# Performance work log

Measured on AMD Instinct MI355X. Metric: run time of the kernel, lower is better.

Reference implementation:

```python
import jax, jax.numpy as jnp
import numpy as np

B, T, F, H, O = 128, 512, 512, 1024, 1


def setup_inputs() -> dict:
    key = jax.random.key(0)
    ks = jax.random.split(key, 11)
    s_ih1 = 1.0 / np.sqrt(H)
    return {
        "x": jax.random.normal(ks[0], (B, T, F), dtype=jnp.float32),
        # LSTMCell params, torch layout: weight_ih [4H, in], weight_hh [4H, H]
        "W_ih1": jax.random.uniform(ks[1], (4 * H, F), jnp.float32, -s_ih1, s_ih1),
        "W_hh1": jax.random.uniform(ks[2], (4 * H, H), jnp.float32, -s_ih1, s_ih1),
        "b_ih1": jax.random.uniform(ks[3], (4 * H,), jnp.float32, -s_ih1, s_ih1),
        "b_hh1": jax.random.uniform(ks[4], (4 * H,), jnp.float32, -s_ih1, s_ih1),
        "W_ih2": jax.random.uniform(ks[5], (4 * H, H), jnp.float32, -s_ih1, s_ih1),
        "W_hh2": jax.random.uniform(ks[6], (4 * H, H), jnp.float32, -s_ih1, s_ih1),
        "b_ih2": jax.random.uniform(ks[7], (4 * H,), jnp.float32, -s_ih1, s_ih1),
        "b_hh2": jax.random.uniform(ks[8], (4 * H,), jnp.float32, -s_ih1, s_ih1),
        "W_lin": jax.random.uniform(ks[9], (O, H), jnp.float32, -s_ih1, s_ih1),
        "b_lin": jax.random.uniform(ks[10], (O,), jnp.float32, -s_ih1, s_ih1),
    }


def _lstm_cell(x_t, h, c, W_ih, W_hh, b_ih, b_hh):
    # gates: [B, 4H]; torch gate order i, f, g, o
    gates = x_t @ W_ih.T + b_ih + h @ W_hh.T + b_hh
    i, f, g, o = jnp.split(gates, 4, axis=-1)
    i, f, o = jax.nn.sigmoid(i), jax.nn.sigmoid(f), jax.nn.sigmoid(o)
    g = jnp.tanh(g)
    c_new = f * c + i * g
    h_new = o * jnp.tanh(c_new)
    return h_new, c_new


def reference(x, W_ih1, W_hh1, b_ih1, b_hh1, W_ih2, W_hh2, b_ih2, b_hh2, W_lin, b_lin):
    B_, dtype = x.shape[0], x.dtype
    zeros = jnp.zeros((B_, H), dtype=dtype)
    init = (zeros, zeros, zeros, zeros)  # h1, c1, h2, c2

    def step(carry, x_t):
        h1, c1, h2, c2 = carry
        h1, c1 = _lstm_cell(x_t, h1, c1, W_ih1, W_hh1, b_ih1, b_hh1)
        h2, c2 = _lstm_cell(h1, h2, c2, W_ih2, W_hh2, b_ih2, b_hh2)
        return (h1, c1, h2, c2), None

    (h1, c1, h2, c2), _ = jax.lax.scan(step, init, jnp.swapaxes(x, 0, 1))
    # linear applied to the last timestep's h2 only (loop overwrites output)
    return h2 @ W_lin.T + b_lin
```

## Files before the change

kernel.cpp:

```cpp
#include <hip/hip_runtime.h>

#define Bb  128
#define Tt  512
#define Ff  512
#define Hh  1024
#define BH  (Bb*Hh)
#define WGS 512
#define NBLK 192

#define OFF_H1   0u
#define OFF_H2   524288u
#define OFF_H2F  1048576u
#define OFF_BAR  1572864u
#define OFF_PB   1576960u
#define OFF_WB   5771264u
#define OFF_XB   9965568u
#define WS_MIN   9965568u
#define WS_FULL  77074432u

typedef __attribute__((ext_vector_type(8))) short short8;
typedef __attribute__((ext_vector_type(4))) float f32x4;

__device__ __forceinline__ short f2bf(float f){
  union { float fv; unsigned u; } v; v.fv = f;
  unsigned r = v.u + 0x7fffu + ((v.u >> 16) & 1u);
  return (short)(r >> 16);
}

__device__ __forceinline__ f32x4 mfma16(short8 a, short8 b, f32x4 c){
  return __builtin_amdgcn_mfma_f32_16x16x32_bf16(a, b, c, 0, 0, 0);
}

#define CLDH(dst, base, OFFB) \
  asm volatile("global_load_dwordx4 %0, %1, off offset:" #OFFB " sc0 sc1" \
               : "=v"(dst) : "v"(base) : "memory")
#define CLDF(dst, base, OFFB) \
  asm volatile("global_load_dwordx4 %0, %1, off offset:" #OFFB " sc0 sc1" \
               : "=v"(dst) : "v"(base) : "memory")
#define CSTF(base, val, OFFB) \
  asm volatile("global_store_dwordx4 %0, %1, off offset:" #OFFB " sc0 sc1" \
               :: "v"(base), "v"(val) : "memory")

__device__ __forceinline__ void st_bf16_coh(short* p, short v){
  asm volatile("global_store_short %0, %1, off sc0 sc1"
               :: "v"(p), "v"((unsigned)(unsigned short)v) : "memory");
}

__global__ void __launch_bounds__(WGS) conv_wih1(const float* __restrict__ W,
                                                 short* __restrict__ Wb){
  const int fi   = blockIdx.x * WGS + threadIdx.x;
  const int nt   = fi >> 10;
  const int ch   = (fi >> 6) & 15;
  const int lane = fi & 63;
  const int grow = nt*16 + (lane & 15);
  const int k    = (ch << 5) + ((lane >> 4) << 3);
  const float* s = W + (size_t)grow * Ff + k;
  short8 v;
  #pragma unroll
  for (int e = 0; e < 8; ++e) v[e] = f2bf(s[e]);
  *(short8*)(Wb + (size_t)fi * 8) = v;
}

__global__ void __launch_bounds__(WGS) conv_x(const float* __restrict__ xf,
                                              short* __restrict__ xb){
  const size_t i = ((size_t)blockIdx.x * WGS + threadIdx.x) * 8;
  float4 u0 = *(const float4*)(xf + i);
  float4 u1 = *(const float4*)(xf + i + 4);
  short8 v;
  v[0]=f2bf(u0.x); v[1]=f2bf(u0.y); v[2]=f2bf(u0.z); v[3]=f2bf(u0.w);
  v[4]=f2bf(u1.x); v[5]=f2bf(u1.y); v[6]=f2bf(u1.z); v[7]=f2bf(u1.w);
  *(short8*)(xb + i) = v;
}

__global__ void __launch_bounds__(WGS) lstm_spec(
    const float* __restrict__ x, const short* __restrict__ xb, int use_xb,
    const float* __restrict__ Whh1,
    const float* __restrict__ bih1, const float* __restrict__ bhh1,
    const float* __restrict__ Wih2, const float* __restrict__ Whh2,
    const float* __restrict__ bih2, const float* __restrict__ bhh2,
    const short* __restrict__ Wb,
    short* __restrict__ h1buf, short* __restrict__ h2buf,
    float* __restrict__ PB, float* __restrict__ h2f32,
    unsigned* __restrict__ bar)
{
  extern __shared__ short LW[];
  const int bid = blockIdx.x, tid = threadIdx.x;
  const int grp = bid >> 6;
  const int cu  = bid & 63;
  const int c0  = cu << 4;

  const float* Wsrc = (grp == 0) ? Whh1 : (grp == 1) ? Wih2 : Whh2;
  for (int fi = tid; fi < 8192; fi += WGS){
    const int g = fi >> 11, ch = (fi >> 6) & 31, ln = fi & 63;
    const int grow = (g << 10) + c0 + (ln & 15);
    const int k    = (ch << 5) + ((ln >> 4) << 3);
    const float* s = Wsrc + (size_t)grow * Hh + k;
    short8 v;
    #pragma unroll
    for (int e = 0; e < 8; ++e) v[e] = f2bf(s[e]);
    *(short8*)(LW + (size_t)fi * 8) = v;
  }
  __syncthreads();

  const int lane = tid & 63, wv = tid >> 6;
  const int r0   = (wv << 4) + (lane & 15);
  const int kg8  = (lane >> 4) << 3;
  const int j    = lane & 15;
  const int bb   = (wv << 4) + ((lane >> 4) << 2);
  const int gcol = c0 + j;
  const int slot = bid & 7;

  float bsum[4], cst[4];
  #pragma unroll
  for (int g = 0; g < 4; ++g)
    bsum[g] = (grp == 0) ? bih1[(g << 10) + gcol] + bhh1[(g << 10) + gcol]
            : (grp == 2) ? bih2[(g << 10) + gcol] + bhh2[(g << 10) + gcol] : 0.f;
  #pragma unroll
  for (int r = 0; r < 4; ++r) cst[r] = 0.f;

  for (int p = 0; p <= Tt + 1; ++p){
    if (grp == 0 && p < Tt){
      f32x4 acc[4] = {{0,0,0,0},{0,0,0,0},{0,0,0,0},{0,0,0,0}};
      const short* hp  = h1buf + ((p + 1) & 1) * BH + r0 * Hh + kg8;
      const short* xbp = xb + ((size_t)r0 * Tt + p) * Ff + kg8;
      const float* xfp = x  + ((size_t)r0 * Tt + p) * Ff + kg8;
      #pragma unroll
      for (int cb = 0; cb < 4; ++cb){
        const short* hc = hp + (cb << 8);
        short8 hb[8];
        CLDH(hb[0], hc, 0);   CLDH(hb[1], hc, 64);  CLDH(hb[2], hc, 128);
        CLDH(hb[3], hc, 192); CLDH(hb[4], hc, 256); CLDH(hb[5], hc, 320);
        CLDH(hb[6], hc, 384); CLDH(hb[7], hc, 448);
        short8 xa[4];
        if (use_xb){
          #pragma unroll
          for (int u = 0; u < 4; ++u)
            xa[u] = *(const short8*)(xbp + (cb << 7) + (u << 5));
        } else {
          #pragma unroll
          for (int u = 0; u < 4; ++u){
            float4 u0 = *(const float4*)(xfp + (cb << 7) + (u << 5));
            float4 u1 = *(const float4*)(xfp + (cb << 7) + (u << 5) + 4);
            xa[u][0]=f2bf(u0.x); xa[u][1]=f2bf(u0.y); xa[u][2]=f2bf(u0.z); xa[u][3]=f2bf(u0.w);
            xa[u][4]=f2bf(u1.x); xa[u][5]=f2bf(u1.y); xa[u][6]=f2bf(u1.z); xa[u][7]=f2bf(u1.w);
          }
        }
        asm volatile("s_waitcnt vmcnt(0)" ::: "memory");
        __builtin_amdgcn_sched_barrier(0);
        #pragma unroll
        for (int g = 0; g < 4; ++g){
          #pragma unroll
          for (int u = 0; u < 8; ++u)
            acc[g] = mfma16(hb[u], *(const short8*)(LW + ((size_t)(((g<<5)+(cb<<3)+u)<<6) + lane)*8), acc[g]);
          #pragma unroll
          for (int u = 0; u < 4; ++u)
            acc[g] = mfma16(xa[u], *(const short8*)(Wb + ((size_t)((((g<<6)+cu)<<4)+(cb<<2)+u)*64 + lane)*8), acc[g]);
        }
      }
      short* hw = h1buf + (p & 1) * BH;
      #pragma unroll
      for (int r = 0; r < 4; ++r){
        float gi = acc[0][r] + bsum[0], gf = acc[1][r] + bsum[1];
        float gg = acc[2][r] + bsum[2], go = acc[3][r] + bsum[3];
        float iv = 1.f/(1.f+__expf(-gi)), fv = 1.f/(1.f+__expf(-gf));
        float gv = tanhf(gg),             ov = 1.f/(1.f+__expf(-go));
        cst[r] = fv * cst[r] + iv * gv;
        st_bf16_coh(hw + (size_t)(bb + r) * Hh + gcol, f2bf(ov * tanhf(cst[r])));
      }
    } else if (grp == 1 && p >= 1 && p <= Tt){
      f32x4 acc[4] = {{0,0,0,0},{0,0,0,0},{0,0,0,0},{0,0,0,0}};
      const short* hp = h1buf + ((p + 1) & 1) * BH + r0 * Hh + kg8;
      #pragma unroll
      for (int cb = 0; cb < 4; ++cb){
        const short* hc = hp + (cb << 8);
        short8 hb[8];
        CLDH(hb[0], hc, 0);   CLDH(hb[1], hc, 64);  CLDH(hb[2], hc, 128);
        CLDH(hb[3], hc, 192); CLDH(hb[4], hc, 256); CLDH(hb[5], hc, 320);
        CLDH(hb[6], hc, 384); CLDH(hb[7], hc, 448);
        asm volatile("s_waitcnt vmcnt(0)" ::: "memory");
        __builtin_amdgcn_sched_barrier(0);
        #pragma unroll
        for (int g = 0; g < 4; ++g)
          #pragma unroll
          for (int u = 0; u < 8; ++u)
            acc[g] = mfma16(hb[u], *(const short8*)(LW + ((size_t)(((g<<5)+(cb<<3)+u)<<6) + lane)*8), acc[g]);
      }
      float* pw = PB + (((size_t)((p + 1) & 1) * 64 + cu) * 8 + wv) * 1024 + lane * 16;
      CSTF(pw, acc[0], 0); CSTF(pw, acc[1], 16); CSTF(pw, acc[2], 32); CSTF(pw, acc[3], 48);
    } else if (grp == 2 && p >= 2){
      const float* pr = PB + (((size_t)(p & 1) * 64 + cu) * 8 + wv) * 1024 + lane * 16;
      f32x4 acc[4];
      CLDF(acc[0], pr, 0); CLDF(acc[1], pr, 16); CLDF(acc[2], pr, 32); CLDF(acc[3], pr, 48);
      const short* hp = h2buf + ((p + 1) & 1) * BH + r0 * Hh + kg8;
      #pragma unroll
      for (int cb = 0; cb < 4; ++cb){
        const short* hc = hp + (cb << 8);
        short8 hb[8];
        CLDH(hb[0], hc, 0);   CLDH(hb[1], hc, 64);  CLDH(hb[2], hc, 128);
        CLDH(hb[3], hc, 192); CLDH(hb[4], hc, 256); CLDH(hb[5], hc, 320);
        CLDH(hb[6], hc, 384); CLDH(hb[7], hc, 448);
        asm volatile("s_waitcnt vmcnt(0)" ::: "memory");
        __builtin_amdgcn_sched_barrier(0);
        #pragma unroll
        for (int g = 0; g < 4; ++g)
          #pragma unroll
          for (int u = 0; u < 8; ++u)
            acc[g] = mfma16(hb[u], *(const short8*)(LW + ((size_t)(((g<<5)+(cb<<3)+u)<<6) + lane)*8), acc[g]);
      }
      short* hw = h2buf + (p & 1) * BH;
      #pragma unroll
      for (int r = 0; r < 4; ++r){
        float gi = acc[0][r] + bsum[0], gf = acc[1][r] + bsum[1];
        float gg = acc[2][r] + bsum[2], go = acc[3][r] + bsum[3];
        float iv = 1.f/(1.f+__expf(-gi)), fv = 1.f/(1.f+__expf(-gf));
        float gv = tanhf(gg),             ov = 1.f/(1.f+__expf(-go));
        cst[r] = fv * cst[r] + iv * gv;
        float hv = ov * tanhf(cst[r]);
        st_bf16_coh(hw + (size_t)(bb + r) * Hh + gcol, f2bf(hv));
        if (p == Tt + 1) h2f32[(size_t)(bb + r) * Hh + gcol] = hv;
      }
    }

    __syncthreads();
    if (tid == 0){
      unsigned prev = __hip_atomic_fetch_add(bar + (slot << 6), 1u,
                        __ATOMIC_RELAXED, __HIP_MEMORY_SCOPE_AGENT);
      if (prev == (unsigned)(24 * (p + 1)) - 1u)
        __hip_atomic_fetch_add(bar + 768, 1u,
                        __ATOMIC_RELAXED, __HIP_MEMORY_SCOPE_AGENT);
      while (__hip_atomic_load(bar + 768,
                        __ATOMIC_RELAXED, __HIP_MEMORY_SCOPE_AGENT)
             < (unsigned)(8 * (p + 1)))
        __builtin_amdgcn_s_sleep(2);
    }
    __syncthreads();
  }
}

__global__ void final_linear(const float* __restrict__ h2, const float* __restrict__ Wl,
                             const float* __restrict__ bl, float* __restrict__ out){
  __shared__ float red[256];
  const int b = blockIdx.x, t = threadIdx.x;
  float s = 0.f;
  for (int k = t; k < Hh; k += 256) s += h2[(size_t)b * Hh + k] * Wl[k];
  red[t] = s; __syncthreads();
  for (int off = 128; off > 0; off >>= 1){ if (t < off) red[t] += red[t + off]; __syncthreads(); }
  if (t == 0) out[b] = red[0] + bl[0];
}

extern "C" void kernel_launch(void* const* d_in, const int* in_sizes, int n_in,
                              void* d_out, int out_size, void* d_ws, size_t ws_size,
                              hipStream_t stream) {
  (void)in_sizes; (void)n_in; (void)out_size;
  const float* x    = (const float*)d_in[0];
  const float* Wih1 = (const float*)d_in[1];
  const float* Whh1 = (const float*)d_in[2];
  const float* bih1 = (const float*)d_in[3];
  const float* bhh1 = (const float*)d_in[4];
  const float* Wih2 = (const float*)d_in[5];
  const float* Whh2 = (const float*)d_in[6];
  const float* bih2 = (const float*)d_in[7];
  const float* bhh2 = (const float*)d_in[8];
  const float* Wlin = (const float*)d_in[9];
  const float* blin = (const float*)d_in[10];
  float* out = (float*)d_out;

  if (ws_size < WS_MIN) return;
  const int use_xb = (ws_size >= WS_FULL) ? 1 : 0;

  char* ws = (char*)d_ws;
  short*    h1buf = (short*)(ws + OFF_H1);
  short*    h2buf = (short*)(ws + OFF_H2);
  float*    h2f32 = (float*)(ws + OFF_H2F);
  unsigned* bar   = (unsigned*)(ws + OFF_BAR);
  float*    PB    = (float*)(ws + OFF_PB);
  short*    Wb    = (short*)(ws + OFF_WB);
  short*    xb    = (short*)(ws + OFF_XB);

  hipMemsetAsync(d_ws, 0, OFF_WB, stream);
  conv_wih1<<<dim3(512), dim3(WGS), 0, stream>>>(Wih1, Wb);
  if (use_xb) conv_x<<<dim3(8192), dim3(WGS), 0, stream>>>(x, xb);
  hipFuncSetAttribute(reinterpret_cast<const void*>(lstm_spec),
                      hipFuncAttributeMaxDynamicSharedMemorySize, 131072);
  lstm_spec<<<dim3(NBLK), dim3(WGS), 131072, stream>>>(
      x, use_xb ? xb : Wb, use_xb, Whh1, bih1, bhh1, Wih2, Whh2, bih2, bhh2,
      Wb, h1buf, h2buf, PB, h2f32, bar);
  final_linear<<<dim3(Bb), dim3(256), 0, stream>>>(h2f32, Wlin, blin, out);
}
```

Before: 11.72 ms.

## Restructure persistent LSTM into four-group pipeline with register-resident weights and 32x32 MFMA

Adds a fourth block group that computes the x·W_ih1 projection one step ahead into a double-buffered PBX array, so it comes off the layer-1 critical path. Weights now sit in registers as bf16 fragments, and hidden states are staged through swizzled LDS for 32x32x16 MFMAs. A K-split with an LDS reduction is added, and gate columns are interleaved so each thread handles all four gates of one unit. The cost is an extra pipeline phase, more global scratch traffic for the preactivations, high register pressure, and mandatory full workspace use.

```diff
diff --git a/kernel.cpp b/kernel.cpp
--- a/kernel.cpp
+++ b/kernel.cpp
@@ -6,59 +6,54 @@
 #define Hh  1024
 #define BH  (Bb*Hh)
 #define WGS 512
-#define NBLK 192
+#define NBLK 256
+#define NPH 515
+#define PBH (128*4096)
 
 #define OFF_H1   0u
 #define OFF_H2   524288u
 #define OFF_H2F  1048576u
 #define OFF_BAR  1572864u
 #define OFF_PB   1576960u
-#define OFF_WB   5771264u
+#define OFF_PBX  5771264u
 #define OFF_XB   9965568u
-#define WS_MIN   9965568u
-#define WS_FULL  77074432u
+#define WS_NEED  77074432u
 
 typedef __attribute__((ext_vector_type(8))) short short8;
 typedef __attribute__((ext_vector_type(4))) float f32x4;
+typedef __attribute__((ext_vector_type(16))) float f32x16;
 
 __device__ __forceinline__ short f2bf(float f){
   union { float fv; unsigned u; } v; v.fv = f;
   unsigned r = v.u + 0x7fffu + ((v.u >> 16) & 1u);
   return (short)(r >> 16);
 }
-
-__device__ __forceinline__ f32x4 mfma16(short8 a, short8 b, f32x4 c){
-  return __builtin_amdgcn_mfma_f32_16x16x32_bf16(a, b, c, 0, 0, 0);
-}
-
-#define CLDH(dst, base, OFFB) \
-  asm volatile("global_load_dwordx4 %0, %1, off offset:" #OFFB " sc0 sc1" \
-               : "=v"(dst) : "v"(base) : "memory")
-#define CLDF(dst, base, OFFB) \
-  asm volatile("global_load_dwordx4 %0, %1, off offset:" #OFFB " sc0 sc1" \
-               : "=v"(dst) : "v"(base) : "memory")
-#define CSTF(base, val, OFFB) \
-  asm volatile("global_store_dwordx4 %0, %1, off offset:" #OFFB " sc0 sc1" \
-               :: "v"(base), "v"(val) : "memory")
-
-__device__ __forceinline__ void st_bf16_coh(short* p, short v){
+__device__ __forceinline__ float sigm(float x){ return 1.f/(1.f+__expf(-x)); }
+
+__device__ __forceinline__ f32x16 mfma32(short8 a, short8 b, f32x16 c){
+  return __builtin_amdgcn_mfma_f32_32x32x16_bf16(a, b, c, 0, 0, 0);
+}
+
+__device__ __forceinline__ short8 scld8(const short* p){
+  short8 d;
+  asm volatile("global_load_dwordx4 %0, %1, off sc0 sc1" : "=v"(d) : "v"(p) : "memory");
+  return d;
+}
+__device__ __forceinline__ f32x4 scldf4(const float* p){
+  f32x4 d;
+  asm volatile("global_load_dwordx4 %0, %1, off sc0 sc1" : "=v"(d) : "v"(p) : "memory");
+  return d;
+}
+__device__ __forceinline__ void sstf4(float* p, f32x4 v){
+  asm volatile("global_store_dwordx4 %0, %1, off sc0 sc1" :: "v"(p), "v"(v) : "memory");
+}
+__device__ __forceinline__ void ssth(short* p, short v){
   asm volatile("global_store_short %0, %1, off sc0 sc1"
                :: "v"(p), "v"((unsigned)(unsigned short)v) : "memory");
 }
-
-__global__ void __launch_bounds__(WGS) conv_wih1(const float* __restrict__ W,
-                                                 short* __restrict__ Wb){
-  const int fi   = blockIdx.x * WGS + threadIdx.x;
-  const int nt   = fi >> 10;
-  const int ch   = (fi >> 6) & 15;
-  const int lane = fi & 63;
-  const int grow = nt*16 + (lane & 15);
-  const int k    = (ch << 5) + ((lane >> 4) << 3);
-  const float* s = W + (size_t)grow * Ff + k;
-  short8 v;
-  #pragma unroll
-  for (int e = 0; e < 8; ++e) v[e] = f2bf(s[e]);
-  *(short8*)(Wb + (size_t)fi * 8) = v;
+__device__ __forceinline__ void drain_vm(){
+  asm volatile("s_waitcnt vmcnt(0)" ::: "memory");
+  __builtin_amdgcn_sched_barrier(0);
 }
 
 __global__ void __launch_bounds__(WGS) conv_x(const float* __restrict__ xf,
@@ -72,166 +67,206 @@
   *(short8*)(xb + i) = v;
 }
 
-__global__ void __launch_bounds__(WGS) lstm_spec(
-    const float* __restrict__ x, const short* __restrict__ xb, int use_xb,
-    const float* __restrict__ Whh1,
+__global__ void __launch_bounds__(WGS, 2) lstm4(
+    const short* __restrict__ xb,
+    const float* __restrict__ Wih1, const float* __restrict__ Whh1,
     const float* __restrict__ bih1, const float* __restrict__ bhh1,
     const float* __restrict__ Wih2, const float* __restrict__ Whh2,
     const float* __restrict__ bih2, const float* __restrict__ bhh2,
-    const short* __restrict__ Wb,
-    short* __restrict__ h1buf, short* __restrict__ h2buf,
-    float* __restrict__ PB, float* __restrict__ h2f32,
-    unsigned* __restrict__ bar)
+    short* __restrict__ h1, short* __restrict__ h2,
+    float* __restrict__ PB, float* __restrict__ PBX,
+    float* __restrict__ h2f32, unsigned* __restrict__ bar)
 {
-  extern __shared__ short LW[];
+  extern __shared__ char lds[];
+  float* F  = (float*)lds;
+  float* Lb = (float*)(lds + 131072);
+
   const int bid = blockIdx.x, tid = threadIdx.x;
   const int grp = bid >> 6;
   const int cu  = bid & 63;
-  const int c0  = cu << 4;
-
-  const float* Wsrc = (grp == 0) ? Whh1 : (grp == 1) ? Wih2 : Whh2;
-  for (int fi = tid; fi < 8192; fi += WGS){
-    const int g = fi >> 11, ch = (fi >> 6) & 31, ln = fi & 63;
-    const int grow = (g << 10) + c0 + (ln & 15);
-    const int k    = (ch << 5) + ((ln >> 4) << 3);
-    const float* s = Wsrc + (size_t)grow * Hh + k;
+  const int c0h = cu << 4;
+  const int lane = tid & 63, wv = tid >> 6;
+  const int tc = lane & 31, hi = lane >> 5;
+  const int slot = bid & 7;
+
+  const int cth = wv & 1;
+  const int kh  = (wv >> 1) & 1;
+  const int rh  = wv >> 2;
+  const int xrt = wv >> 1;
+
+  if (tid < 64){
+    const int hc = tid >> 2, g = tid & 3;
+    float v = 0.f;
+    if (grp == 0) v = bih1[(g<<10) + c0h + hc] + bhh1[(g<<10) + c0h + hc];
+    if (grp == 2) v = bih2[(g<<10) + c0h + hc] + bhh2[(g<<10) + c0h + hc];
+    Lb[tid] = v;
+  }
+
+  const float* Wsrc = (grp==0) ? Whh1 : (grp==1) ? Wih2 : (grp==2) ? Whh2 : Wih1;
+  const int Kdim = (grp==3) ? Ff : Hh;
+  const int kb0  = (grp==3) ? 0 : kh*512;
+  const int wrow = (tc&3)*Hh + c0h + cth*8 + (tc>>2);
+  short8 bfr[32];
+  #pragma unroll
+  for (int f = 0; f < 32; ++f){
+    const float* s = Wsrc + (size_t)wrow*Kdim + kb0 + f*16 + hi*8;
+    float4 u0 = *(const float4*)(s);
+    float4 u1 = *(const float4*)(s + 4);
     short8 v;
-    #pragma unroll
-    for (int e = 0; e < 8; ++e) v[e] = f2bf(s[e]);
-    *(short8*)(LW + (size_t)fi * 8) = v;
+    v[0]=f2bf(u0.x); v[1]=f2bf(u0.y); v[2]=f2bf(u0.z); v[3]=f2bf(u0.w);
+    v[4]=f2bf(u1.x); v[5]=f2bf(u1.y); v[6]=f2bf(u1.z); v[7]=f2bf(u1.w);
+    bfr[f] = v;
   }
   __syncthreads();
 
-  const int lane = tid & 63, wv = tid >> 6;
-  const int r0   = (wv << 4) + (lane & 15);
-  const int kg8  = (lane >> 4) << 3;
-  const int j    = lane & 15;
-  const int bb   = (wv << 4) + ((lane >> 4) << 2);
-  const int gcol = c0 + j;
-  const int slot = bid & 7;
-
-  float bsum[4], cst[4];
-  #pragma unroll
-  for (int g = 0; g < 4; ++g)
-    bsum[g] = (grp == 0) ? bih1[(g << 10) + gcol] + bhh1[(g << 10) + gcol]
-            : (grp == 2) ? bih2[(g << 10) + gcol] + bhh2[(g << 10) + gcol] : 0.f;
-  #pragma unroll
-  for (int r = 0; r < 4; ++r) cst[r] = 0.f;
-
-  for (int p = 0; p <= Tt + 1; ++p){
-    if (grp == 0 && p < Tt){
-      f32x4 acc[4] = {{0,0,0,0},{0,0,0,0},{0,0,0,0},{0,0,0,0}};
-      const short* hp  = h1buf + ((p + 1) & 1) * BH + r0 * Hh + kg8;
-      const short* xbp = xb + ((size_t)r0 * Tt + p) * Ff + kg8;
-      const float* xfp = x  + ((size_t)r0 * Tt + p) * Ff + kg8;
+  float cst[4] = {0.f, 0.f, 0.f, 0.f};
+  const int swz = (lane & 31) << 4;
+
+  for (int p = 0; p < NPH; ++p){
+    const bool act = (grp==0) ? (p>=1 && p<=512)
+                   : (grp==1) ? (p>=2 && p<=513)
+                   : (grp==2) ? (p>=3 && p<=514)
+                   :            (p < 512);
+    const short* sh = (grp==2) ? (h2 + (p&1)*BH) : (h1 + (p&1)*BH);
+
+    f32x4 pre[4] = {{0,0,0,0},{0,0,0,0},{0,0,0,0},{0,0,0,0}};
+    if (act && (grp == 0 || grp == 2)){
+      const float* src = (grp == 0) ? (PBX + (size_t)((p+1)&1)*PBH)
+                                    : (PB  + (size_t)((p+1)&1)*PBH);
       #pragma unroll
-      for (int cb = 0; cb < 4; ++cb){
-        const short* hc = hp + (cb << 8);
-        short8 hb[8];
-        CLDH(hb[0], hc, 0);   CLDH(hb[1], hc, 64);  CLDH(hb[2], hc, 128);
-        CLDH(hb[3], hc, 192); CLDH(hb[4], hc, 256); CLDH(hb[5], hc, 320);
-        CLDH(hb[6], hc, 384); CLDH(hb[7], hc, 448);
-        short8 xa[4];
-        if (use_xb){
-          #pragma unroll
-          for (int u = 0; u < 4; ++u)
-            xa[u] = *(const short8*)(xbp + (cb << 7) + (u << 5));
+      for (int s4 = 0; s4 < 4; ++s4){
+        const int id = (s4<<9) + tid;
+        pre[s4] = scldf4(src + (size_t)(id>>4)*4096 + ((c0h + (id&15))<<2));
+      }
+    }
+
+    f32x16 a0, a1;
+    #pragma unroll
+    for (int i = 0; i < 16; ++i){ a0[i] = 0.f; a1[i] = 0.f; }
+
+    #pragma unroll
+    for (int r = 0; r < 2; ++r){
+      if (act){
+        if (grp != 3){
+          #pragma unroll
+          for (int buf = 0; buf < 2; ++buf){
+            const int kq = 2*buf + r;
+            short8 t[8];
+            #pragma unroll
+            for (int i = 0; i < 8; ++i){
+              const int u = (i<<9) + tid;
+              t[i] = scld8(sh + (size_t)(u>>5)*Hh + kq*256 + (u&31)*8);
+            }
+            drain_vm();
+            #pragma unroll
+            for (int i = 0; i < 8; ++i){
+              const int u = (i<<9) + tid;
+              *(short8*)(lds + buf*65536 + (((u<<4)) ^ ((((u>>5)&31))<<4))) = t[i];
+            }
+          }
         } else {
-          #pragma unroll
-          for (int u = 0; u < 4; ++u){
-            float4 u0 = *(const float4*)(xfp + (cb << 7) + (u << 5));
-            float4 u1 = *(const float4*)(xfp + (cb << 7) + (u << 5) + 4);
-            xa[u][0]=f2bf(u0.x); xa[u][1]=f2bf(u0.y); xa[u][2]=f2bf(u0.z); xa[u][3]=f2bf(u0.w);
-            xa[u][4]=f2bf(u1.x); xa[u][5]=f2bf(u1.y); xa[u][6]=f2bf(u1.z); xa[u][7]=f2bf(u1.w);
-          }
-        }
-        asm volatile("s_waitcnt vmcnt(0)" ::: "memory");
-        __builtin_amdgcn_sched_barrier(0);
+          short8 t[8];
+          #pragma unroll
+          for (int i = 0; i < 8; ++i){
+            const int u = (i<<9) + tid;
+            t[i] = *(const short8*)(xb + ((size_t)(u>>5)*Tt + p)*Ff + r*256 + (u&31)*8);
+          }
+          #pragma unroll
+          for (int i = 0; i < 8; ++i){
+            const int u = (i<<9) + tid;
+            *(short8*)(lds + r*65536 + (((u<<4)) ^ ((((u>>5)&31))<<4))) = t[i];
+          }
+        }
+      }
+      __syncthreads();
+      if (act){
+        if (grp != 3){
+          const int row0 = rh*64 + (lane & 31);
+          const char* b0 = lds + kh*65536 + row0*512;
+          const char* b1 = b0 + 32*512;
+          #pragma unroll
+          for (int ci = 0; ci < 16; ++ci){
+            const int ko = (((ci<<5) | (hi<<4)) ^ swz);
+            short8 A0 = *(const short8*)(b0 + ko);
+            short8 A1 = *(const short8*)(b1 + ko);
+            a0 = mfma32(A0, bfr[r*16+ci], a0);
+            a1 = mfma32(A1, bfr[r*16+ci], a1);
+          }
+        } else {
+          const int row0 = xrt*32 + (lane & 31);
+          const char* b0 = lds + r*65536 + row0*512;
+          #pragma unroll
+          for (int ci = 0; ci < 16; ++ci){
+            const int ko = (((ci<<5) | (hi<<4)) ^ swz);
+            short8 A0 = *(const short8*)(b0 + ko);
+            a0 = mfma32(A0, bfr[r*16+ci], a0);
+          }
+        }
+      }
+      __syncthreads();
+    }
+
+    if (act){
+      const int colf = (cth<<5) + tc;
+      if (grp != 3){
         #pragma unroll
-        for (int g = 0; g < 4; ++g){
-          #pragma unroll
-          for (int u = 0; u < 8; ++u)
-            acc[g] = mfma16(hb[u], *(const short8*)(LW + ((size_t)(((g<<5)+(cb<<3)+u)<<6) + lane)*8), acc[g]);
-          #pragma unroll
-          for (int u = 0; u < 4; ++u)
-            acc[g] = mfma16(xa[u], *(const short8*)(Wb + ((size_t)((((g<<6)+cu)<<4)+(cb<<2)+u)*64 + lane)*8), acc[g]);
-        }
-      }
-      short* hw = h1buf + (p & 1) * BH;
+        for (int rg = 0; rg < 16; ++rg){
+          const int rl = (rg&3) + ((rg>>2)<<3) + (hi<<2);
+          F[(kh*128 + rh*64 + rl)*68 + colf]      = a0[rg];
+          F[(kh*128 + rh*64 + 32 + rl)*68 + colf] = a1[rg];
+        }
+      } else {
+        #pragma unroll
+        for (int rg = 0; rg < 16; ++rg){
+          const int rl = (rg&3) + ((rg>>2)<<3) + (hi<<2);
+          F[(xrt*32 + rl)*68 + colf] = a0[rg];
+        }
+      }
+    }
+    __syncthreads();
+
+    if (act){
       #pragma unroll
-      for (int r = 0; r < 4; ++r){
-        float gi = acc[0][r] + bsum[0], gf = acc[1][r] + bsum[1];
-        float gg = acc[2][r] + bsum[2], go = acc[3][r] + bsum[3];
-        float iv = 1.f/(1.f+__expf(-gi)), fv = 1.f/(1.f+__expf(-gf));
-        float gv = tanhf(gg),             ov = 1.f/(1.f+__expf(-go));
-        cst[r] = fv * cst[r] + iv * gv;
-        st_bf16_coh(hw + (size_t)(bb + r) * Hh + gcol, f2bf(ov * tanhf(cst[r])));
-      }
-    } else if (grp == 1 && p >= 1 && p <= Tt){
-      f32x4 acc[4] = {{0,0,0,0},{0,0,0,0},{0,0,0,0},{0,0,0,0}};
-      const short* hp = h1buf + ((p + 1) & 1) * BH + r0 * Hh + kg8;
-      #pragma unroll
-      for (int cb = 0; cb < 4; ++cb){
-        const short* hc = hp + (cb << 8);
-        short8 hb[8];
-        CLDH(hb[0], hc, 0);   CLDH(hb[1], hc, 64);  CLDH(hb[2], hc, 128);
-        CLDH(hb[3], hc, 192); CLDH(hb[4], hc, 256); CLDH(hb[5], hc, 320);
-        CLDH(hb[6], hc, 384); CLDH(hb[7], hc, 448);
-        asm volatile("s_waitcnt vmcnt(0)" ::: "memory");
-        __builtin_amdgcn_sched_barrier(0);
-        #pragma unroll
-        for (int g = 0; g < 4; ++g)
-          #pragma unroll
-          for (int u = 0; u < 8; ++u)
-            acc[g] = mfma16(hb[u], *(const short8*)(LW + ((size_t)(((g<<5)+(cb<<3)+u)<<6) + lane)*8), acc[g]);
-      }
-      float* pw = PB + (((size_t)((p + 1) & 1) * 64 + cu) * 8 + wv) * 1024 + lane * 16;
-      CSTF(pw, acc[0], 0); CSTF(pw, acc[1], 16); CSTF(pw, acc[2], 32); CSTF(pw, acc[3], 48);
-    } else if (grp == 2 && p >= 2){
-      const float* pr = PB + (((size_t)(p & 1) * 64 + cu) * 8 + wv) * 1024 + lane * 16;
-      f32x4 acc[4];
-      CLDF(acc[0], pr, 0); CLDF(acc[1], pr, 16); CLDF(acc[2], pr, 32); CLDF(acc[3], pr, 48);
-      const short* hp = h2buf + ((p + 1) & 1) * BH + r0 * Hh + kg8;
-      #pragma unroll
-      for (int cb = 0; cb < 4; ++cb){
-        const short* hc = hp + (cb << 8);
-        short8 hb[8];
-        CLDH(hb[0], hc, 0);   CLDH(hb[1], hc, 64);  CLDH(hb[2], hc, 128);
-        CLDH(hb[3], hc, 192); CLDH(hb[4], hc, 256); CLDH(hb[5], hc, 320);
-        CLDH(hb[6], hc, 384); CLDH(hb[7], hc, 448);
-        asm volatile("s_waitcnt vmcnt(0)" ::: "memory");
-        __builtin_amdgcn_sched_barrier(0);
-        #pragma unroll
-        for (int g = 0; g < 4; ++g)
-          #pragma unroll
-          for (int u = 0; u < 8; ++u)
-            acc[g] = mfma16(hb[u], *(const short8*)(LW + ((size_t)(((g<<5)+(cb<<3)+u)<<6) + lane)*8), acc[g]);
-      }
-      short* hw = h2buf + (p & 1) * BH;
-      #pragma unroll
-      for (int r = 0; r < 4; ++r){
-        float gi = acc[0][r] + bsum[0], gf = acc[1][r] + bsum[1];
-        float gg = acc[2][r] + bsum[2], go = acc[3][r] + bsum[3];
-        float iv = 1.f/(1.f+__expf(-gi)), fv = 1.f/(1.f+__expf(-gf));
-        float gv = tanhf(gg),             ov = 1.f/(1.f+__expf(-go));
-        cst[r] = fv * cst[r] + iv * gv;
-        float hv = ov * tanhf(cst[r]);
-        st_bf16_coh(hw + (size_t)(bb + r) * Hh + gcol, f2bf(hv));
-        if (p == Tt + 1) h2f32[(size_t)(bb + r) * Hh + gcol] = hv;
+      for (int s = 0; s < 4; ++s){
+        const int id  = (s<<9) + tid;
+        const int row = id >> 4, hc = id & 15;
+        const int gc4 = (c0h + hc) << 2;
+        f32x4 q = *(f32x4*)&F[row*68 + (hc<<2)];
+        if (grp != 3) q += *(f32x4*)&F[(128+row)*68 + (hc<<2)];
+        if (grp == 0){
+          f32x4 bb = *(f32x4*)&Lb[hc<<2];
+          float gi=q[0]+pre[s][0]+bb[0], gf=q[1]+pre[s][1]+bb[1];
+          float gg=q[2]+pre[s][2]+bb[2], go=q[3]+pre[s][3]+bb[3];
+          float iv=sigm(gi), fv=sigm(gf), gv=tanhf(gg), ov=sigm(go);
+          cst[s] = fv*cst[s] + iv*gv;
+          ssth(h1 + ((p+1)&1)*BH + row*Hh + c0h + hc, f2bf(ov*tanhf(cst[s])));
+        } else if (grp == 1){
+          sstf4(PB + (size_t)(p&1)*PBH + row*4096 + gc4, q);
+        } else if (grp == 2){
+          f32x4 bb = *(f32x4*)&Lb[hc<<2];
+          float gi=q[0]+pre[s][0]+bb[0], gf=q[1]+pre[s][1]+bb[1];
+          float gg=q[2]+pre[s][2]+bb[2], go=q[3]+pre[s][3]+bb[3];
+          float iv=sigm(gi), fv=sigm(gf), gv=tanhf(gg), ov=sigm(go);
+          cst[s] = fv*cst[s] + iv*gv;
+          float hv = ov*tanhf(cst[s]);
+          ssth(h2 + ((p+1)&1)*BH + row*Hh + c0h + hc, f2bf(hv));
+          if (p == 514) h2f32[row*Hh + c0h + hc] = hv;
+        } else {
+          sstf4(PBX + (size_t)(p&1)*PBH + row*4096 + gc4, q);
+        }
       }
     }
 
     __syncthreads();
     if (tid == 0){
-      unsigned prev = __hip_atomic_fetch_add(bar + (slot << 6), 1u,
+      unsigned prev = __hip_atomic_fetch_add(bar + (slot<<6), 1u,
                         __ATOMIC_RELAXED, __HIP_MEMORY_SCOPE_AGENT);
-      if (prev == (unsigned)(24 * (p + 1)) - 1u)
+      if (prev == 32u*(p+1) - 1u)
         __hip_atomic_fetch_add(bar + 768, 1u,
                         __ATOMIC_RELAXED, __HIP_MEMORY_SCOPE_AGENT);
       while (__hip_atomic_load(bar + 768,
-                        __ATOMIC_RELAXED, __HIP_MEMORY_SCOPE_AGENT)
-             < (unsigned)(8 * (p + 1)))
-        __builtin_amdgcn_s_sleep(2);
+                        __ATOMIC_RELAXED, __HIP_MEMORY_SCOPE_AGENT) < 8u*(p+1))
+        __builtin_amdgcn_s_sleep(1);
     }
     __syncthreads();
   }
@@ -242,9 +277,9 @@
   __shared__ float red[256];
   const int b = blockIdx.x, t = threadIdx.x;
   float s = 0.f;
-  for (int k = t; k < Hh; k += 256) s += h2[(size_t)b * Hh + k] * Wl[k];
+  for (int k = t; k < Hh; k += 256) s += h2[(size_t)b*Hh + k] * Wl[k];
   red[t] = s; __syncthreads();
-  for (int off = 128; off > 0; off >>= 1){ if (t < off) red[t] += red[t + off]; __syncthreads(); }
+  for (int off = 128; off > 0; off >>= 1){ if (t < off) red[t] += red[t+off]; __syncthreads(); }
   if (t == 0) out[b] = red[0] + bl[0];
 }
 
@@ -265,25 +300,22 @@
   const float* blin = (const float*)d_in[10];
   float* out = (float*)d_out;
 
-  if (ws_size < WS_MIN) return;
-  const int use_xb = (ws_size >= WS_FULL) ? 1 : 0;
-
+  if (ws_size < WS_NEED) return;
   char* ws = (char*)d_ws;
-  short*    h1buf = (short*)(ws + OFF_H1);
-  short*    h2buf = (short*)(ws + OFF_H2);
+  short*    h1b   = (short*)(ws + OFF_H1);
+  short*    h2b   = (short*)(ws + OFF_H2);
   float*    h2f32 = (float*)(ws + OFF_H2F);
   unsigned* bar   = (unsigned*)(ws + OFF_BAR);
   float*    PB    = (float*)(ws + OFF_PB);
-  short*    Wb    = (short*)(ws + OFF_WB);
+  float*    PBX   = (float*)(ws + OFF_PBX);
   short*    xb    = (short*)(ws + OFF_XB);
 
-  hipMemsetAsync(d_ws, 0, OFF_WB, stream);
-  conv_wih1<<<dim3(512), dim3(WGS), 0, stream>>>(Wih1, Wb);
-  if (use_xb) conv_x<<<dim3(8192), dim3(WGS), 0, stream>>>(x, xb);
-  hipFuncSetAttribute(reinterpret_cast<const void*>(lstm_spec),
-                      hipFuncAttributeMaxDynamicSharedMemorySize, 131072);
-  lstm_spec<<<dim3(NBLK), dim3(WGS), 131072, stream>>>(
-      x, use_xb ? xb : Wb, use_xb, Whh1, bih1, bhh1, Wih2, Whh2, bih2, bhh2,
-      Wb, h1buf, h2buf, PB, h2f32, bar);
+  hipMemsetAsync(d_ws, 0, OFF_PB, stream);
+  conv_x<<<dim3(8192), dim3(WGS), 0, stream>>>(x, xb);
+  hipFuncSetAttribute(reinterpret_cast<const void*>(lstm4),
+                      hipFuncAttributeMaxDynamicSharedMemorySize, 131584);
+  lstm4<<<dim3(NBLK), dim3(WGS), 131584, stream>>>(
+      xb, Wih1, Whh1, bih1, bhh1, Wih2, Whh2, bih2, bhh2,
+      h1b, h2b, PB, PBX, h2f32, bar);
   final_linear<<<dim3(Bb), dim3(256), 0, stream>>>(h2f32, Wlin, blin, out);
 }
```

New measurement: 9.456 ms. 19.4% less time.
